# Kernel tuning notes

Hardware: AMD Instinct MI355X
Metric: run time of the kernel (lower is better)

The kernel has to match this reference:

```python
import jax, jax.numpy as jnp
import numpy as np

NUM_ITER = 5
ALPHA = 5.0   # spatial bandwidth, bilateral kernel
BETA = 5.0    # feature bandwidth, bilateral kernel
GAMMA = 5.0   # spatial bandwidth, spatial kernel
W_1 = 1.0
W_2 = 1.0


def setup_inputs() -> dict:
    key = jax.random.key(0)
    k1, k2 = jax.random.split(key)
    B, C, X, Y, Z = 1, 4, 32, 16, 16
    log_unary = jax.random.normal(k1, (B, C, X, Y, Z), dtype=jnp.float32)
    features_pairwise = jax.random.normal(k2, (B, 2, X, Y, Z), dtype=jnp.float32)
    # Potts-model compatibility: ones minus identity, [C_out, C_in] (conv1d kernel size 1)
    compatibility_weights = (jnp.ones((C, C)) - jnp.eye(C)).astype(jnp.float32)
    return {"log_unary": log_unary, "features_pairwise": features_pairwise,
            "compatibility_weights": compatibility_weights}


def _gauss_kernel(f):
    # f: [B, D, N] feature vectors; dense Gaussian filter matrix K_ij = exp(-||f_i-f_j||^2/2)
    sq = jnp.sum(f * f, axis=1)  # [B, N]
    d2 = sq[:, :, None] + sq[:, None, :] - 2.0 * jnp.einsum('bdn,bdm->bnm', f, f)
    return jnp.exp(-0.5 * jnp.maximum(d2, 0.0))  # [B, N, N]


def reference(log_unary, features_pairwise, compatibility_weights):
    B, C, X, Y, Z = log_unary.shape
    N = X * Y * Z
    lu = log_unary.reshape(B, C, N)
    q = jax.nn.softmax(lu, axis=1)

    gx, gy, gz = jnp.meshgrid(jnp.arange(X), jnp.arange(Y), jnp.arange(Z), indexing='ij')
    spatial = jnp.stack([gx, gy, gz], axis=0).astype(jnp.float32).reshape(1, 3, N)
    spatial = jnp.broadcast_to(spatial, (B, 3, N))
    img_fea = features_pairwise.reshape(B, features_pairwise.shape[1], N)

    f1 = jnp.concatenate([spatial / ALPHA, img_fea / BETA], axis=1)  # bilateral features
    f2 = spatial / GAMMA                                             # spatial features

    K1 = _gauss_kernel(f1)
    K2 = _gauss_kernel(f2)
    # norm = filter(ones) = row sums; scale = rsqrt(norm)
    scale1 = jax.lax.rsqrt(jnp.sum(K1, axis=2))[:, None, :]  # [B,1,N]
    scale2 = jax.lax.rsqrt(jnp.sum(K2, axis=2))[:, None, :]

    for _ in range(NUM_ITER):
        q1 = jnp.einsum('bnm,bcm->bcn', K1, q * scale1) * scale1
        q2 = jnp.einsum('bnm,bcm->bcn', K2, q * scale2) * scale2
        q_comb = W_1 * q1 + W_2 * q2
        q_update = jnp.einsum('oc,bcn->bon', compatibility_weights, q_comb)
        q = jax.nn.softmax(lu - q_update, axis=1)

    return q.reshape(B, C, X, Y, Z)
```

## Files before the change

### kernel.cpp

```cpp
#include <hip/hip_runtime.h>
#include <math.h>


constexpr int   NT    = 8192;
constexpr float LOG2E = 1.4426950408889634f;
constexpr float SQL2E = 1.2011224087864498f;
constexpr float INVA  = 0.2f * SQL2E;

constexpr int R_M = 0, R_U1 = 32, R_U2 = 36, R_S1 = 40, R_S2 = 41, R_CV = 42;

static __device__ __forceinline__ float ex2(float x) {
    return __builtin_amdgcn_exp2f(x);
}

__constant__ float INVSQF[7] = {1.f, 1.f, 0.70710678f, 0.40824829f,
                                0.20412415f, 0.09128709f, 0.03726780f};
__constant__ int AB_A[28] = {0, 1,0, 2,1,0, 3,2,1,0, 4,3,2,1,0,
                             5,4,3,2,1,0, 6,5,4,3,2,1,0};
__constant__ int AB_B[28] = {0, 0,1, 0,1,2, 0,1,2,3, 0,1,2,3,4,
                             0,1,2,3,4,5, 0,1,2,3,4,5,6};

static __device__ __forceinline__ void conv3d_store512(float* SP,
                                                       float* __restrict__ outp,
                                                       int tid) {
    float g32[32];
#pragma unroll
    for (int d = 0; d < 32; d++) { float t = d * INVA; g32[d] = ex2(-0.5f*t*t); }
    __syncthreads();
    {
        int r = tid;
        float v[16], acc[16];
#pragma unroll
        for (int z = 0; z < 16; z++) { v[z] = SP[r*17 + z]; acc[z] = 0.f; }
#pragma unroll
        for (int zp = 0; zp < 16; zp++)
#pragma unroll
            for (int z = 0; z < 16; z++) {
                int d = (z > zp) ? (z - zp) : (zp - z);
                acc[z] = fmaf(g32[d], v[zp], acc[z]);
            }
#pragma unroll
        for (int z = 0; z < 16; z++) SP[r*17 + z] = acc[z];
    }
    __syncthreads();
    {
        int x = tid >> 4, z = tid & 15;
        int base = x * 272 + z;
        float v[16], acc[16];
#pragma unroll
        for (int y = 0; y < 16; y++) { v[y] = SP[base + y*17]; acc[y] = 0.f; }
#pragma unroll
        for (int yp = 0; yp < 16; yp++)
#pragma unroll
            for (int y = 0; y < 16; y++) {
                int d = (y > yp) ? (y - yp) : (yp - y);
                acc[y] = fmaf(g32[d], v[yp], acc[y]);
            }
#pragma unroll
        for (int y = 0; y < 16; y++) SP[base + y*17] = acc[y];
    }
    __syncthreads();
    {
        int c = tid & 255, h = tid >> 8;
        int base = (c >> 4) * 17 + (c & 15);
        float v[32];
#pragma unroll
        for (int xp = 0; xp < 32; xp++) v[xp] = SP[base + xp*272];
        float acc[16];
#pragma unroll
        for (int x0 = 0; x0 < 16; x0++) acc[x0] = 0.f;
        if (h == 0) {
#pragma unroll
            for (int xp = 0; xp < 32; xp++)
#pragma unroll
                for (int x0 = 0; x0 < 16; x0++) {
                    int d = (x0 > xp) ? (x0 - xp) : (xp - x0);
                    acc[x0] = fmaf(g32[d], v[xp], acc[x0]);
                }
#pragma unroll
            for (int x0 = 0; x0 < 16; x0++) outp[x0*256 + c] = acc[x0];
        } else {
#pragma unroll
            for (int xp = 0; xp < 32; xp++)
#pragma unroll
                for (int x0 = 0; x0 < 16; x0++) {
                    int x = x0 + 16;
                    int d = (x > xp) ? (x - xp) : (xp - x);
                    acc[x0] = fmaf(g32[d], v[xp], acc[x0]);
                }
#pragma unroll
            for (int x0 = 0; x0 < 16; x0++) outp[(x0+16)*256 + c] = acc[x0];
        }
    }
}

__global__ __launch_bounds__(512) void k_phaseA(const float* __restrict__ feat,
                                                float* __restrict__ W) {
    __shared__ float SP[512 * 17];
    const int bid = blockIdx.x, tid = threadIdx.x;
    const int a = AB_A[bid], b = AB_B[bid];
    const float ca = INVSQF[a], cb = INVSQF[b];
    for (int s = tid; s < NT; s += 512) {
        float g0 = feat[s] * 0.2f, g1 = feat[NT + s] * 0.2f;
        float eg = ex2(-0.5f * LOG2E * (g0*g0 + g1*g1));
        float pa = 1.f;
        for (int i = 0; i < a; i++) pa *= g0;
        float pb = 1.f;
        for (int i = 0; i < b; i++) pb *= g1;
        float v = eg * pa * ca * pb * cb;
        W[(R_M + bid)*NT + s] = v;
        SP[(s >> 4)*17 + (s & 15)] = v;
    }
    conv3d_store512(SP, W + (R_CV + bid)*NT, tid);
}

__global__ __launch_bounds__(256) void k_init(float* __restrict__ W,
                                              const float* __restrict__ lu) {
    int n = blockIdx.x * 256 + threadIdx.x;
    int x = n >> 8, y = (n >> 4) & 15, z = n & 15;
    float Sx = 0.f, Sy = 0.f, Sz = 0.f;
    for (int j = 0; j < 32; j++) { float d = (float)(x-j)*INVA; Sx += ex2(-0.5f*d*d); }
    for (int j = 0; j < 16; j++) { float d = (float)(y-j)*INVA; Sy += ex2(-0.5f*d*d); }
    for (int j = 0; j < 16; j++) { float d = (float)(z-j)*INVA; Sz += ex2(-0.5f*d*d); }
    float s2 = rsqrtf(Sx * Sy * Sz);
    W[R_S2*NT + n] = s2;
    float rs = 0.f;
#pragma unroll
    for (int ab = 0; ab < 28; ab++)
        rs = fmaf(W[(R_M+ab)*NT + n], W[(R_CV+ab)*NT + n], rs);
    float s1 = rsqrtf(rs);
    W[R_S1*NT + n] = s1;
    float l0 = lu[n], l1 = lu[NT+n], l2 = lu[2*NT+n], l3 = lu[3*NT+n];
    float mx = fmaxf(fmaxf(l0,l1), fmaxf(l2,l3));
    float q0 = __expf(l0-mx), q1 = __expf(l1-mx), q2 = __expf(l2-mx), q3 = __expf(l3-mx);
    float inv = 1.f / (q0+q1+q2+q3);
    q0*=inv; q1*=inv; q2*=inv; q3*=inv;
    W[(R_U1+0)*NT+n]=q0*s1; W[(R_U1+1)*NT+n]=q1*s1; W[(R_U1+2)*NT+n]=q2*s1; W[(R_U1+3)*NT+n]=q3*s1;
    W[(R_U2+0)*NT+n]=q0*s2; W[(R_U2+1)*NT+n]=q1*s2; W[(R_U2+2)*NT+n]=q2*s2; W[(R_U2+3)*NT+n]=q3*s2;
}

__global__ __launch_bounds__(512) void k_conv(const float* __restrict__ W,
                                              float* __restrict__ Wout) {
    __shared__ float SP[512 * 17];
    const int idx = blockIdx.x;
    const int tid = threadIdx.x;
    if (idx < 112) {
        const float4* M4 = (const float4*)(W + (R_M + (idx >> 2))*NT);
        const float4* U4 = (const float4*)(W + (R_U1 + (idx & 3))*NT);
#pragma unroll
        for (int i = 0; i < 4; i++) {
            int s4 = tid + i*512;
            float4 m = M4[s4], u = U4[s4];
            int s = s4 << 2;
            int base = (s >> 4)*17 + (s & 15);
            SP[base+0] = m.x*u.x; SP[base+1] = m.y*u.y;
            SP[base+2] = m.z*u.z; SP[base+3] = m.w*u.w;
        }
    } else {
        const float4* U4 = (const float4*)(W + (R_U2 + (idx - 112))*NT);
#pragma unroll
        for (int i = 0; i < 4; i++) {
            int s4 = tid + i*512;
            float4 u = U4[s4];
            int s = s4 << 2;
            int base = (s >> 4)*17 + (s & 15);
            SP[base+0] = u.x; SP[base+1] = u.y; SP[base+2] = u.z; SP[base+3] = u.w;
        }
    }
    conv3d_store512(SP, Wout + (R_CV + idx)*NT, tid);
}

__global__ __launch_bounds__(256) void k_fuse(float* __restrict__ W,
        const float* __restrict__ lu, const float* __restrict__ compat,
        float* __restrict__ out, int last) {
    int n = blockIdx.x * 256 + threadIdx.x;
    float s1 = W[R_S1*NT + n], s2 = W[R_S2*NT + n];
    float q1[4] = {0.f, 0.f, 0.f, 0.f};
#pragma unroll
    for (int ab = 0; ab < 28; ab++) {
        float m = W[(R_M+ab)*NT + n];
#pragma unroll
        for (int c = 0; c < 4; c++)
            q1[c] = fmaf(m, W[(R_CV + ab*4 + c)*NT + n], q1[c]);
    }
    float comb[4];
#pragma unroll
    for (int c = 0; c < 4; c++)
        comb[c] = s1 * q1[c] + s2 * W[(R_CV + 112 + c)*NT + n];
    float q[4];
#pragma unroll
    for (int o = 0; o < 4; o++) {
        float upd = 0.f;
#pragma unroll
        for (int c = 0; c < 4; c++) upd = fmaf(compat[o*4+c], comb[c], upd);
        q[o] = lu[o*NT+n] - upd;
    }
    float mx = fmaxf(fmaxf(q[0],q[1]), fmaxf(q[2],q[3]));
    float sum = 0.f;
#pragma unroll
    for (int c = 0; c < 4; c++) { q[c] = __expf(q[c]-mx); sum += q[c]; }
    float inv = 1.f / sum;
    if (last) {
#pragma unroll
        for (int c = 0; c < 4; c++) out[c*NT+n] = q[c] * inv;
    } else {
#pragma unroll
        for (int c = 0; c < 4; c++) {
            float qq = q[c] * inv;
            W[(R_U1+c)*NT+n] = qq*s1;
            W[(R_U2+c)*NT+n] = qq*s2;
        }
    }
}

extern "C" void kernel_launch(void* const* d_in, const int* in_sizes, int n_in,
                              void* d_out, int out_size, void* d_ws, size_t ws_size,
                              hipStream_t stream) {
    const float* lu     = (const float*)d_in[0];
    const float* feat   = (const float*)d_in[1];
    const float* compat = (const float*)d_in[2];
    float* out = (float*)d_out;
    float* W   = (float*)d_ws;

    k_phaseA<<<dim3(28),  dim3(512), 0, stream>>>(feat, W);
    k_init  <<<dim3(32),  dim3(256), 0, stream>>>(W, lu);
    for (int it = 0; it < 5; it++) {
        k_conv<<<dim3(116), dim3(512), 0, stream>>>(W, W);
        k_fuse<<<dim3(32),  dim3(256), 0, stream>>>(W, lu, compat, out, it == 4);
    }
}
```

Baseline: 139.6 us.

## Fold output weights into conv epilogue and move spatial norm into phaseA

The conv epilogue now multiplies each convolved value by its per-voxel weights (M times s1 for the bilateral terms, s2 for the spatial term) before storing. k_fuse and k_init therefore only sum the rows instead of doing FMA with M, which removes 28 M-plane reads per voxel in each fuse pass. The spatial normalisation s2 is now computed by four extra blocks of k_phaseA, taking that work out of k_init. In exchange, each conv thread reads one or two extra global arrays in its store loop, and k_phaseA launches more blocks.

```diff
diff --git a/kernel.cpp b/kernel.cpp
--- a/kernel.cpp
+++ b/kernel.cpp
@@ -22,6 +22,8 @@
 
 static __device__ __forceinline__ void conv3d_store512(float* SP,
                                                        float* __restrict__ outp,
+                                                       const float* w0,
+                                                       const float* w1,
                                                        int tid) {
     float g32[32];
 #pragma unroll
@@ -78,7 +80,12 @@
                     acc[x0] = fmaf(g32[d], v[xp], acc[x0]);
                 }
 #pragma unroll
-            for (int x0 = 0; x0 < 16; x0++) outp[x0*256 + c] = acc[x0];
+            for (int x0 = 0; x0 < 16; x0++) {
+                int n = x0*256 + c;
+                float w = w0 ? w0[n] : 1.f;
+                if (w1) w *= w1[n];
+                outp[n] = w * acc[x0];
+            }
         } else {
 #pragma unroll
             for (int xp = 0; xp < 32; xp++)
@@ -89,7 +96,12 @@
                     acc[x0] = fmaf(g32[d], v[xp], acc[x0]);
                 }
 #pragma unroll
-            for (int x0 = 0; x0 < 16; x0++) outp[(x0+16)*256 + c] = acc[x0];
+            for (int x0 = 0; x0 < 16; x0++) {
+                int n = (x0+16)*256 + c;
+                float w = w0 ? w0[n] : 1.f;
+                if (w1) w *= w1[n];
+                outp[n] = w * acc[x0];
+            }
         }
     }
 }
@@ -98,37 +110,44 @@
                                                 float* __restrict__ W) {
     __shared__ float SP[512 * 17];
     const int bid = blockIdx.x, tid = threadIdx.x;
-    const int a = AB_A[bid], b = AB_B[bid];
-    const float ca = INVSQF[a], cb = INVSQF[b];
-    for (int s = tid; s < NT; s += 512) {
-        float g0 = feat[s] * 0.2f, g1 = feat[NT + s] * 0.2f;
-        float eg = ex2(-0.5f * LOG2E * (g0*g0 + g1*g1));
-        float pa = 1.f;
-        for (int i = 0; i < a; i++) pa *= g0;
-        float pb = 1.f;
-        for (int i = 0; i < b; i++) pb *= g1;
-        float v = eg * pa * ca * pb * cb;
-        W[(R_M + bid)*NT + s] = v;
-        SP[(s >> 4)*17 + (s & 15)] = v;
-    }
-    conv3d_store512(SP, W + (R_CV + bid)*NT, tid);
+    if (bid < 28) {
+        const int a = AB_A[bid], b = AB_B[bid];
+        const float ca = INVSQF[a], cb = INVSQF[b];
+        for (int s = tid; s < NT; s += 512) {
+            float g0 = feat[s] * 0.2f, g1 = feat[NT + s] * 0.2f;
+            float eg = ex2(-0.5f * LOG2E * (g0*g0 + g1*g1));
+            float pa = 1.f;
+            for (int i = 0; i < a; i++) pa *= g0;
+            float pb = 1.f;
+            for (int i = 0; i < b; i++) pb *= g1;
+            float v = eg * pa * ca * pb * cb;
+            W[(R_M + bid)*NT + s] = v;
+            SP[(s >> 4)*17 + (s & 15)] = v;
+        }
+        conv3d_store512(SP, W + (R_CV + bid)*NT, W + (R_M + bid)*NT, nullptr, tid);
+    } else {
+#pragma unroll
+        for (int i = 0; i < 4; i++) {
+            int n = (bid - 28) * 2048 + i*512 + tid;
+            int x = n >> 8, y = (n >> 4) & 15, z = n & 15;
+            float Sx = 0.f, Sy = 0.f, Sz = 0.f;
+            for (int j = 0; j < 32; j++) { float d = (float)(x-j)*INVA; Sx += ex2(-0.5f*d*d); }
+            for (int j = 0; j < 16; j++) { float d = (float)(y-j)*INVA; Sy += ex2(-0.5f*d*d); }
+            for (int j = 0; j < 16; j++) { float d = (float)(z-j)*INVA; Sz += ex2(-0.5f*d*d); }
+            W[R_S2*NT + n] = rsqrtf(Sx * Sy * Sz);
+        }
+    }
 }
 
 __global__ __launch_bounds__(256) void k_init(float* __restrict__ W,
                                               const float* __restrict__ lu) {
     int n = blockIdx.x * 256 + threadIdx.x;
-    int x = n >> 8, y = (n >> 4) & 15, z = n & 15;
-    float Sx = 0.f, Sy = 0.f, Sz = 0.f;
-    for (int j = 0; j < 32; j++) { float d = (float)(x-j)*INVA; Sx += ex2(-0.5f*d*d); }
-    for (int j = 0; j < 16; j++) { float d = (float)(y-j)*INVA; Sy += ex2(-0.5f*d*d); }
-    for (int j = 0; j < 16; j++) { float d = (float)(z-j)*INVA; Sz += ex2(-0.5f*d*d); }
-    float s2 = rsqrtf(Sx * Sy * Sz);
-    W[R_S2*NT + n] = s2;
     float rs = 0.f;
 #pragma unroll
     for (int ab = 0; ab < 28; ab++)
-        rs = fmaf(W[(R_M+ab)*NT + n], W[(R_CV+ab)*NT + n], rs);
+        rs += W[(R_CV+ab)*NT + n];
     float s1 = rsqrtf(rs);
+    float s2 = W[R_S2*NT + n];
     W[R_S1*NT + n] = s1;
     float l0 = lu[n], l1 = lu[NT+n], l2 = lu[2*NT+n], l3 = lu[3*NT+n];
     float mx = fmaxf(fmaxf(l0,l1), fmaxf(l2,l3));
@@ -156,6 +175,8 @@
             SP[base+0] = m.x*u.x; SP[base+1] = m.y*u.y;
             SP[base+2] = m.z*u.z; SP[base+3] = m.w*u.w;
         }
+        conv3d_store512(SP, Wout + (R_CV + idx)*NT,
+                        W + (R_M + (idx >> 2))*NT, W + R_S1*NT, tid);
     } else {
         const float4* U4 = (const float4*)(W + (R_U2 + (idx - 112))*NT);
 #pragma unroll
@@ -166,27 +187,23 @@
             int base = (s >> 4)*17 + (s & 15);
             SP[base+0] = u.x; SP[base+1] = u.y; SP[base+2] = u.z; SP[base+3] = u.w;
         }
-    }
-    conv3d_store512(SP, Wout + (R_CV + idx)*NT, tid);
+        conv3d_store512(SP, Wout + (R_CV + idx)*NT, W + R_S2*NT, nullptr, tid);
+    }
 }
 
 __global__ __launch_bounds__(256) void k_fuse(float* __restrict__ W,
         const float* __restrict__ lu, const float* __restrict__ compat,
         float* __restrict__ out, int last) {
     int n = blockIdx.x * 256 + threadIdx.x;
-    float s1 = W[R_S1*NT + n], s2 = W[R_S2*NT + n];
-    float q1[4] = {0.f, 0.f, 0.f, 0.f};
-#pragma unroll
-    for (int ab = 0; ab < 28; ab++) {
-        float m = W[(R_M+ab)*NT + n];
+    float comb[4] = {0.f, 0.f, 0.f, 0.f};
+#pragma unroll
+    for (int ab = 0; ab < 28; ab++)
 #pragma unroll
         for (int c = 0; c < 4; c++)
-            q1[c] = fmaf(m, W[(R_CV + ab*4 + c)*NT + n], q1[c]);
-    }
-    float comb[4];
+            comb[c] += W[(R_CV + ab*4 + c)*NT + n];
 #pragma unroll
     for (int c = 0; c < 4; c++)
-        comb[c] = s1 * q1[c] + s2 * W[(R_CV + 112 + c)*NT + n];
+        comb[c] += W[(R_CV + 112 + c)*NT + n];
     float q[4];
 #pragma unroll
     for (int o = 0; o < 4; o++) {
@@ -204,6 +221,7 @@
 #pragma unroll
         for (int c = 0; c < 4; c++) out[c*NT+n] = q[c] * inv;
     } else {
+        float s1 = W[R_S1*NT + n], s2 = W[R_S2*NT + n];
 #pragma unroll
         for (int c = 0; c < 4; c++) {
             float qq = q[c] * inv;
@@ -222,7 +240,7 @@
     float* out = (float*)d_out;
     float* W   = (float*)d_ws;
 
-    k_phaseA<<<dim3(28),  dim3(512), 0, stream>>>(feat, W);
+    k_phaseA<<<dim3(32),  dim3(512), 0, stream>>>(feat, W);
     k_init  <<<dim3(32),  dim3(256), 0, stream>>>(W, lu);
     for (int it = 0; it < 5; it++) {
         k_conv<<<dim3(116), dim3(512), 0, stream>>>(W, W);
```

Result: faster. 131.1 us (-6.1%).
